# Kernel tuning notes

Measured on AMD Instinct MI355X. Metric: run time of the kernel, lower is better.

Reference implementation:

```python
import jax, jax.numpy as jnp
import numpy as np

D_PRIME = 512
D = 2048
CLASSES = 4


def setup_inputs() -> dict:
    key = jax.random.key(0)
    k1, k2, k3, k4 = jax.random.split(key, 4)
    N = 32768
    V_prime = jax.random.normal(k1, (N, D), dtype=jnp.float32)
    U_t = jax.random.normal(k2, (D_PRIME, D), dtype=jnp.float32)
    W_mta = jax.random.normal(k3, (1, D_PRIME), dtype=jnp.float32)
    W = jax.random.normal(k4, (CLASSES, D), dtype=jnp.float32)
    return {"V_prime": V_prime, "U_t": U_t, "W_mta": W_mta, "W": W}


def reference(V_prime, U_t, W_mta, W):
    # [D_prime, N] = tanh(U_t @ V'^T)
    tanh_scores = jnp.tanh(U_t @ V_prime.T)
    # attention over instances: [1, N]
    a = jax.nn.softmax(W_mta @ tanh_scores, axis=1)
    # weighted sum pooling: [D]
    t = jnp.sum(a.T * V_prime, axis=0)
    # final linear: [1, classes]
    l = (W @ t).reshape(1, CLASSES)
    return l
```

## Files before the change

kernel.cpp:

```cpp
#include <hip/hip_runtime.h>

#define N_INST 32768
#define DIM    2048
#define DP     512
#define NCLS   4

typedef _Float16 half8_t __attribute__((ext_vector_type(8)));
typedef float    float4_t __attribute__((ext_vector_type(4)));

#define OFF_UHI   0ull
#define OFF_S     (OFF_UHI  + (size_t)DP*DIM*2)
#define OFF_STAT  (OFF_S    + (size_t)N_INST*4)
#define OFF_PSTAT (OFF_STAT + 256ull)
#define OFF_PART  (OFF_PSTAT+ 256ull)

__device__ __forceinline__ float tanh_fast(float x) {
  float e = __expf(2.0f * x);
  return 1.0f - 2.0f / (e + 1.0f);
}

__global__ __launch_bounds__(256) void k_cvt(const float4* __restrict__ in,
                                             half8_t* __restrict__ out) {
  int i = blockIdx.x * 256 + threadIdx.x;
  float4 a = in[2 * i], b = in[2 * i + 1];
  half8_t h;
  h[0] = (_Float16)a.x; h[1] = (_Float16)a.y;
  h[2] = (_Float16)a.z; h[3] = (_Float16)a.w;
  h[4] = (_Float16)b.x; h[5] = (_Float16)b.y;
  h[6] = (_Float16)b.z; h[7] = (_Float16)b.w;
  out[i] = h;
}

__global__ __launch_bounds__(256) void k_score_gemm(
    const _Float16* __restrict__ Uhi, const float* __restrict__ V,
    const float* __restrict__ Wmta, float* __restrict__ s) {
  __shared__ _Float16 lA[128 * 32];
  __shared__ _Float16 lB[128 * 32];

  const int tid = threadIdx.x;
  const int lane = tid & 63;
  const int wv = tid >> 6;
  const int waveM = wv >> 1;
  const int waveN = wv & 1;
  const int quad = lane >> 4;
  const int col = lane & 15;

  const int b = blockIdx.x;
  const int grp = b >> 5;
  const int win = b & 31;
  const int mb = win >> 3;
  const int nb = grp * 8 + (win & 7);

  const int aRow0 = mb * 128;
  const int bRow0 = nb * 128;
  const int kStart = (nb & 63) << 5;

  float4_t acc[4][4];
  const float4_t z4 = {0.f, 0.f, 0.f, 0.f};
  for (int i = 0; i < 4; i++)
    for (int j = 0; j < 4; j++) acc[i][j] = z4;

  const int stR = tid >> 2;
  const int stQ = (tid & 3) << 3;

  const _Float16* gA0 = Uhi + (size_t)(aRow0 + stR) * DIM + stQ;
  const _Float16* gA1 = Uhi + (size_t)(aRow0 + 64 + stR) * DIM + stQ;
  const float*    gB0 = V   + (size_t)(bRow0 + stR) * DIM + stQ;
  const float*    gB1 = V   + (size_t)(bRow0 + 64 + stR) * DIM + stQ;

  uint4  ra0, ra1;
  float4 rb0a, rb0b, rb1a, rb1b;

  ra0 = *(const uint4*)(gA0 + kStart);  ra1 = *(const uint4*)(gA1 + kStart);
  rb0a = *(const float4*)(gB0 + kStart);  rb0b = *(const float4*)(gB0 + kStart + 4);
  rb1a = *(const float4*)(gB1 + kStart);  rb1b = *(const float4*)(gB1 + kStart + 4);

  for (int ki = 0; ki < 64; ++ki) {
    __syncthreads();
    *(uint4*)&lA[stR * 32 + stQ] = ra0;
    *(uint4*)&lA[(stR + 64) * 32 + stQ] = ra1;
    {
      half8_t h0, h1;
      h0[0] = (_Float16)rb0a.x; h0[1] = (_Float16)rb0a.y;
      h0[2] = (_Float16)rb0a.z; h0[3] = (_Float16)rb0a.w;
      h0[4] = (_Float16)rb0b.x; h0[5] = (_Float16)rb0b.y;
      h0[6] = (_Float16)rb0b.z; h0[7] = (_Float16)rb0b.w;
      h1[0] = (_Float16)rb1a.x; h1[1] = (_Float16)rb1a.y;
      h1[2] = (_Float16)rb1a.z; h1[3] = (_Float16)rb1a.w;
      h1[4] = (_Float16)rb1b.x; h1[5] = (_Float16)rb1b.y;
      h1[6] = (_Float16)rb1b.z; h1[7] = (_Float16)rb1b.w;
      *(half8_t*)&lB[stR * 32 + stQ] = h0;
      *(half8_t*)&lB[(stR + 64) * 32 + stQ] = h1;
    }
    __syncthreads();

    const int kp = (kStart + (ki + 1) * 32) & (DIM - 1);
    ra0 = *(const uint4*)(gA0 + kp);  ra1 = *(const uint4*)(gA1 + kp);
    rb0a = *(const float4*)(gB0 + kp);  rb0b = *(const float4*)(gB0 + kp + 4);
    rb1a = *(const float4*)(gB1 + kp);  rb1b = *(const float4*)(gB1 + kp + 4);

    half8_t af[4], bf[4];
    for (int mi = 0; mi < 4; mi++) {
      const int row = waveM * 64 + mi * 16 + col;
      af[mi] = *(const half8_t*)&lA[row * 32 + quad * 8];
    }
    for (int ni = 0; ni < 4; ni++) {
      const int row = waveN * 64 + ni * 16 + col;
      bf[ni] = *(const half8_t*)&lB[row * 32 + quad * 8];
    }
    for (int mi = 0; mi < 4; mi++)
      for (int ni = 0; ni < 4; ni++)
        acc[mi][ni] = __builtin_amdgcn_mfma_f32_16x16x32_f16(af[mi], bf[ni], acc[mi][ni], 0, 0, 0);
  }

  for (int ni = 0; ni < 4; ni++) {
    float v = 0.0f;
    for (int mi = 0; mi < 4; mi++) {
      const int jb = aRow0 + waveM * 64 + mi * 16 + quad * 4;
      union { float4_t v4; float f[4]; } u;
      u.v4 = acc[mi][ni];
      for (int r = 0; r < 4; r++)
        v += Wmta[jb + r] * tanh_fast(u.f[r]);
    }
    v += __shfl_xor(v, 16);
    v += __shfl_xor(v, 32);
    if (quad == 0) {
      const int n = bRow0 + waveN * 64 + ni * 16 + col;
      atomicAdd(&s[n], v);
    }
  }
}

__global__ __launch_bounds__(256) void k_stats1(const float* __restrict__ s,
                                                float* __restrict__ pstat) {
  const int tid = threadIdx.x;
  const int lane = tid & 63;
  const int wvi = tid >> 6;
  __shared__ float smM[4], smP[4];
  const float4* s4 = (const float4*)s;

  float4 v = s4[blockIdx.x * 256 + tid];
  float m = fmaxf(fmaxf(v.x, v.y), fmaxf(v.z, v.w));
  float p = __expf(v.x - m) + __expf(v.y - m) + __expf(v.z - m) + __expf(v.w - m);
  for (int o = 32; o > 0; o >>= 1) {
    float om = __shfl_xor(m, o);
    float op = __shfl_xor(p, o);
    float nm = fmaxf(m, om);
    p = p * __expf(m - nm) + op * __expf(om - nm);
    m = nm;
  }
  if (lane == 0) { smM[wvi] = m; smP[wvi] = p; }
  __syncthreads();
  if (tid == 0) {
    float gm = fmaxf(fmaxf(smM[0], smM[1]), fmaxf(smM[2], smM[3]));
    float sum = 0.f;
    for (int w = 0; w < 4; w++) sum += smP[w] * __expf(smM[w] - gm);
    pstat[blockIdx.x * 2]     = gm;
    pstat[blockIdx.x * 2 + 1] = sum;
  }
}

__global__ __launch_bounds__(64) void k_stats2(const float* __restrict__ pstat,
                                               float* __restrict__ stats) {
  const int tid = threadIdx.x;
  float m = -3.4e38f, p = 0.0f;
  if (tid < 32) { m = pstat[tid * 2]; p = pstat[tid * 2 + 1]; }
  for (int o = 32; o > 0; o >>= 1) {
    float om = __shfl_xor(m, o);
    float op = __shfl_xor(p, o);
    float nm = fmaxf(m, om);
    p = p * __expf(m - nm) + op * __expf(om - nm);
    m = nm;
  }
  if (tid == 0) { stats[0] = m; stats[1] = 1.0f / p; }
}

__global__ __launch_bounds__(256) void k_pool(const float* __restrict__ V,
                                              const float* __restrict__ s,
                                              const float* __restrict__ stats,
                                              float* __restrict__ part) {
  const int tid = threadIdx.x;
  const float mx = stats[0], inv = stats[1];
  const int n0 = blockIdx.x * 128;
  float acc[8] = {0.f, 0.f, 0.f, 0.f, 0.f, 0.f, 0.f, 0.f};
  for (int r = 0; r < 128; ++r) {
    const int n = n0 + r;
    const float w = __expf(s[n] - mx) * inv;
    if (w > 1e-12f) {
      const float4* vp = (const float4*)&V[(size_t)n * DIM + tid * 8];
      float4 va = vp[0], vb = vp[1];
      acc[0] += w * va.x; acc[1] += w * va.y; acc[2] += w * va.z; acc[3] += w * va.w;
      acc[4] += w * vb.x; acc[5] += w * vb.y; acc[6] += w * vb.z; acc[7] += w * vb.w;
    }
  }
  float* dst = &part[(size_t)blockIdx.x * DIM + tid * 8];
  *(float4*)(dst + 0) = make_float4(acc[0], acc[1], acc[2], acc[3]);
  *(float4*)(dst + 4) = make_float4(acc[4], acc[5], acc[6], acc[7]);
}

__global__ __launch_bounds__(256) void k_reduce_final(const float* __restrict__ part,
                                                      const float* __restrict__ W,
                                                      float* __restrict__ out) {
  const int d = blockIdx.x * 256 + threadIdx.x;
  float t = 0.f;
  for (int bb = 0; bb < 256; ++bb) t += part[(size_t)bb * DIM + d];

  float pc[NCLS];
#pragma unroll
  for (int c = 0; c < NCLS; ++c) pc[c] = W[(size_t)c * DIM + d] * t;

  __shared__ float sred[4][NCLS];
  const int lane = threadIdx.x & 63;
  const int wvi = threadIdx.x >> 6;
#pragma unroll
  for (int c = 0; c < NCLS; ++c)
    for (int o = 32; o > 0; o >>= 1) pc[c] += __shfl_xor(pc[c], o);
  if (lane == 0)
    for (int c = 0; c < NCLS; ++c) sred[wvi][c] = pc[c];
  __syncthreads();
  if (threadIdx.x < NCLS) {
    float v = sred[0][threadIdx.x] + sred[1][threadIdx.x] +
              sred[2][threadIdx.x] + sred[3][threadIdx.x];
    atomicAdd(&out[threadIdx.x], v);
  }
}

extern "C" void kernel_launch(void* const* d_in, const int* in_sizes, int n_in,
                              void* d_out, int out_size, void* d_ws, size_t ws_size,
                              hipStream_t stream) {
  const float* Vp   = (const float*)d_in[0];
  const float* Ut   = (const float*)d_in[1];
  const float* Wmta = (const float*)d_in[2];
  const float* W    = (const float*)d_in[3];
  float* out = (float*)d_out;

  char* ws = (char*)d_ws;
  _Float16* Uhi  = (_Float16*)(ws + OFF_UHI);
  float*    sBuf = (float*)(ws + OFF_S);
  float*    stat = (float*)(ws + OFF_STAT);
  float*    pstat= (float*)(ws + OFF_PSTAT);
  float*    partB= (float*)(ws + OFF_PART);

  hipMemsetAsync(sBuf, 0, (size_t)N_INST * 4, stream);
  hipMemsetAsync(out, 0, (size_t)NCLS * 4, stream);

  k_cvt<<<(DP * DIM / 8) / 256, 256, 0, stream>>>((const float4*)Ut, (half8_t*)Uhi);
  k_score_gemm<<<(DP / 128) * (N_INST / 128), 256, 0, stream>>>(Uhi, Vp, Wmta, sBuf);
  k_stats1<<<32, 256, 0, stream>>>(sBuf, pstat);
  k_stats2<<<1, 64, 0, stream>>>(pstat, stat);
  k_pool<<<N_INST / 128, 256, 0, stream>>>(Vp, sBuf, stat, partB);
  k_reduce_final<<<DIM / 256, 256, 0, stream>>>(partB, W, out);
}
```

Baseline: 492.1 us.

## Load GEMM tiles directly to LDS and fuse pool reduction via atomics

After: 537.4 us. +9.2%, slower.

```diff
diff --git a/kernel.cpp b/kernel.cpp
--- a/kernel.cpp
+++ b/kernel.cpp
@@ -5,18 +5,24 @@
 #define DP     512
 #define NCLS   4
 
-typedef _Float16 half8_t __attribute__((ext_vector_type(8)));
+typedef _Float16 half8_t  __attribute__((ext_vector_type(8)));
 typedef float    float4_t __attribute__((ext_vector_type(4)));
 
 #define OFF_UHI   0ull
 #define OFF_S     (OFF_UHI  + (size_t)DP*DIM*2)
 #define OFF_STAT  (OFF_S    + (size_t)N_INST*4)
 #define OFF_PSTAT (OFF_STAT + 256ull)
-#define OFF_PART  (OFF_PSTAT+ 256ull)
+#define OFF_T     (OFF_PSTAT+ 256ull)
 
 __device__ __forceinline__ float tanh_fast(float x) {
   float e = __expf(2.0f * x);
   return 1.0f - 2.0f / (e + 1.0f);
+}
+
+typedef const unsigned int __attribute__((address_space(1)))* gas_t;
+typedef unsigned int       __attribute__((address_space(3)))* las_t;
+__device__ __forceinline__ void gl16(const void* g, void* l) {
+  __builtin_amdgcn_global_load_lds((gas_t)g, (las_t)l, 16, 0, 0);
 }
 
 __global__ __launch_bounds__(256) void k_cvt(const float4* __restrict__ in,
@@ -35,90 +41,111 @@
     const _Float16* __restrict__ Uhi, const float* __restrict__ V,
     const float* __restrict__ Wmta, float* __restrict__ s) {
   __shared__ _Float16 lA[128 * 32];
-  __shared__ _Float16 lB[128 * 32];
-
-  const int tid = threadIdx.x;
+  __shared__ float    lB[128 * 32];
+
+  const int tid  = threadIdx.x;
   const int lane = tid & 63;
-  const int wv = tid >> 6;
+  const int wv   = tid >> 6;
   const int waveM = wv >> 1;
   const int waveN = wv & 1;
   const int quad = lane >> 4;
-  const int col = lane & 15;
-
-  const int b = blockIdx.x;
+  const int col  = lane & 15;
+
+  const int b   = blockIdx.x;
   const int grp = b >> 5;
   const int win = b & 31;
-  const int mb = win >> 3;
-  const int nb = grp * 8 + (win & 7);
-
-  const int aRow0 = mb * 128;
-  const int bRow0 = nb * 128;
+  const int mb  = win >> 3;
+  const int nb  = grp * 8 + (win & 7);
+
+  const int aRow0  = mb * 128;
+  const int bRow0  = nb * 128;
   const int kStart = (nb & 63) << 5;
+
+  const int rA0 = wv * 32 + (lane >> 2);
+  const int sA  = (lane & 3) ^ ((rA0 >> 1) & 3);
+  const _Float16* gA0 = Uhi + (size_t)(aRow0 + rA0) * DIM + sA * 8;
+  const _Float16* gA1 = gA0 + (size_t)16 * DIM;
+  _Float16* lAd0 = &lA[(wv * 2 + 0) * 512];
+  _Float16* lAd1 = &lA[(wv * 2 + 1) * 512];
+
+  const int rB0 = wv * 32 + (lane >> 3);
+  const int sB  = (lane & 7) ^ (rB0 & 7);
+  const float* gB0 = V + (size_t)(bRow0 + rB0) * DIM + sB * 4;
+  const float* gB1 = gB0 + (size_t)8  * DIM;
+  const float* gB2 = gB0 + (size_t)16 * DIM;
+  const float* gB3 = gB0 + (size_t)24 * DIM;
+  float* lBd0 = &lB[(wv * 4 + 0) * 256];
+  float* lBd1 = &lB[(wv * 4 + 1) * 256];
+  float* lBd2 = &lB[(wv * 4 + 2) * 256];
+  float* lBd3 = &lB[(wv * 4 + 3) * 256];
+
+  int offA[4];
+#pragma unroll
+  for (int mi = 0; mi < 4; ++mi) {
+    const int r = waveM * 64 + mi * 16 + col;
+    offA[mi] = r * 64 + ((quad ^ ((r >> 1) & 3)) << 4);
+  }
+  int offB[4];
+#pragma unroll
+  for (int ni = 0; ni < 4; ++ni) {
+    const int r = waveN * 64 + ni * 16 + col;
+    offB[ni] = r * 128 + ((((quad << 1)) ^ (r & 7)) << 4);
+  }
 
   float4_t acc[4][4];
   const float4_t z4 = {0.f, 0.f, 0.f, 0.f};
+#pragma unroll
   for (int i = 0; i < 4; i++)
+#pragma unroll
     for (int j = 0; j < 4; j++) acc[i][j] = z4;
 
-  const int stR = tid >> 2;
-  const int stQ = (tid & 3) << 3;
-
-  const _Float16* gA0 = Uhi + (size_t)(aRow0 + stR) * DIM + stQ;
-  const _Float16* gA1 = Uhi + (size_t)(aRow0 + 64 + stR) * DIM + stQ;
-  const float*    gB0 = V   + (size_t)(bRow0 + stR) * DIM + stQ;
-  const float*    gB1 = V   + (size_t)(bRow0 + 64 + stR) * DIM + stQ;
-
-  uint4  ra0, ra1;
-  float4 rb0a, rb0b, rb1a, rb1b;
-
-  ra0 = *(const uint4*)(gA0 + kStart);  ra1 = *(const uint4*)(gA1 + kStart);
-  rb0a = *(const float4*)(gB0 + kStart);  rb0b = *(const float4*)(gB0 + kStart + 4);
-  rb1a = *(const float4*)(gB1 + kStart);  rb1b = *(const float4*)(gB1 + kStart + 4);
+  const char* lAc = (const char*)lA;
+  const char* lBc = (const char*)lB;
 
   for (int ki = 0; ki < 64; ++ki) {
+    const int k = (kStart + (ki << 5)) & (DIM - 1);
     __syncthreads();
-    *(uint4*)&lA[stR * 32 + stQ] = ra0;
-    *(uint4*)&lA[(stR + 64) * 32 + stQ] = ra1;
-    {
-      half8_t h0, h1;
-      h0[0] = (_Float16)rb0a.x; h0[1] = (_Float16)rb0a.y;
-      h0[2] = (_Float16)rb0a.z; h0[3] = (_Float16)rb0a.w;
-      h0[4] = (_Float16)rb0b.x; h0[5] = (_Float16)rb0b.y;
-      h0[6] = (_Float16)rb0b.z; h0[7] = (_Float16)rb0b.w;
-      h1[0] = (_Float16)rb1a.x; h1[1] = (_Float16)rb1a.y;
-      h1[2] = (_Float16)rb1a.z; h1[3] = (_Float16)rb1a.w;
-      h1[4] = (_Float16)rb1b.x; h1[5] = (_Float16)rb1b.y;
-      h1[6] = (_Float16)rb1b.z; h1[7] = (_Float16)rb1b.w;
-      *(half8_t*)&lB[stR * 32 + stQ] = h0;
-      *(half8_t*)&lB[(stR + 64) * 32 + stQ] = h1;
-    }
+    gl16(gA0 + k, lAd0);
+    gl16(gA1 + k, lAd1);
+    gl16(gB0 + k, lBd0);
+    gl16(gB1 + k, lBd1);
+    gl16(gB2 + k, lBd2);
+    gl16(gB3 + k, lBd3);
     __syncthreads();
 
-    const int kp = (kStart + (ki + 1) * 32) & (DIM - 1);
-    ra0 = *(const uint4*)(gA0 + kp);  ra1 = *(const uint4*)(gA1 + kp);
-    rb0a = *(const float4*)(gB0 + kp);  rb0b = *(const float4*)(gB0 + kp + 4);
-    rb1a = *(const float4*)(gB1 + kp);  rb1b = *(const float4*)(gB1 + kp + 4);
-
-    half8_t af[4], bf[4];
-    for (int mi = 0; mi < 4; mi++) {
-      const int row = waveM * 64 + mi * 16 + col;
-      af[mi] = *(const half8_t*)&lA[row * 32 + quad * 8];
-    }
-    for (int ni = 0; ni < 4; ni++) {
-      const int row = waveN * 64 + ni * 16 + col;
-      bf[ni] = *(const half8_t*)&lB[row * 32 + quad * 8];
-    }
-    for (int mi = 0; mi < 4; mi++)
-      for (int ni = 0; ni < 4; ni++)
-        acc[mi][ni] = __builtin_amdgcn_mfma_f32_16x16x32_f16(af[mi], bf[ni], acc[mi][ni], 0, 0, 0);
-  }
-
+    half8_t af[4];
+#pragma unroll
+    for (int mi = 0; mi < 4; ++mi)
+      af[mi] = *(const half8_t*)(lAc + offA[mi]);
+
+#pragma unroll
+    for (int ni = 0; ni < 4; ++ni) {
+      const float4_t x = *(const float4_t*)(lBc + offB[ni]);
+      const float4_t y = *(const float4_t*)(lBc + (offB[ni] ^ 16));
+      const auto c0 = __builtin_amdgcn_cvt_pkrtz(x[0], x[1]);
+      const auto c1 = __builtin_amdgcn_cvt_pkrtz(x[2], x[3]);
+      const auto c2 = __builtin_amdgcn_cvt_pkrtz(y[0], y[1]);
+      const auto c3 = __builtin_amdgcn_cvt_pkrtz(y[2], y[3]);
+      half8_t bf;
+      bf[0] = (_Float16)c0[0]; bf[1] = (_Float16)c0[1];
+      bf[2] = (_Float16)c1[0]; bf[3] = (_Float16)c1[1];
+      bf[4] = (_Float16)c2[0]; bf[5] = (_Float16)c2[1];
+      bf[6] = (_Float16)c3[0]; bf[7] = (_Float16)c3[1];
+#pragma unroll
+      for (int mi = 0; mi < 4; ++mi)
+        acc[mi][ni] = __builtin_amdgcn_mfma_f32_16x16x32_f16(af[mi], bf, acc[mi][ni], 0, 0, 0);
+    }
+  }
+
+#pragma unroll
   for (int ni = 0; ni < 4; ni++) {
     float v = 0.0f;
+#pragma unroll
     for (int mi = 0; mi < 4; mi++) {
       const int jb = aRow0 + waveM * 64 + mi * 16 + quad * 4;
       union { float4_t v4; float f[4]; } u;
       u.v4 = acc[mi][ni];
+#pragma unroll
       for (int r = 0; r < 4; r++)
         v += Wmta[jb + r] * tanh_fast(u.f[r]);
     }
@@ -178,51 +205,61 @@
 __global__ __launch_bounds__(256) void k_pool(const float* __restrict__ V,
                                               const float* __restrict__ s,
                                               const float* __restrict__ stats,
-                                              float* __restrict__ part) {
-  const int tid = threadIdx.x;
+                                              float* __restrict__ t) {
+  __shared__ float wsm[128];
+  __shared__ int hot;
+  const int tid = threadIdx.x;
+  if (tid == 0) hot = 0;
+  __syncthreads();
   const float mx = stats[0], inv = stats[1];
   const int n0 = blockIdx.x * 128;
+  if (tid < 128) {
+    const float w = __expf(s[n0 + tid] - mx) * inv;
+    wsm[tid] = w;
+    if (w > 1e-12f) atomicOr(&hot, 1);
+  }
+  __syncthreads();
+  if (hot == 0) return;
+
   float acc[8] = {0.f, 0.f, 0.f, 0.f, 0.f, 0.f, 0.f, 0.f};
   for (int r = 0; r < 128; ++r) {
-    const int n = n0 + r;
-    const float w = __expf(s[n] - mx) * inv;
+    const float w = wsm[r];
     if (w > 1e-12f) {
-      const float4* vp = (const float4*)&V[(size_t)n * DIM + tid * 8];
+      const float4* vp = (const float4*)&V[(size_t)(n0 + r) * DIM + tid * 8];
       float4 va = vp[0], vb = vp[1];
       acc[0] += w * va.x; acc[1] += w * va.y; acc[2] += w * va.z; acc[3] += w * va.w;
       acc[4] += w * vb.x; acc[5] += w * vb.y; acc[6] += w * vb.z; acc[7] += w * vb.w;
     }
   }
-  float* dst = &part[(size_t)blockIdx.x * DIM + tid * 8];
-  *(float4*)(dst + 0) = make_float4(acc[0], acc[1], acc[2], acc[3]);
-  *(float4*)(dst + 4) = make_float4(acc[4], acc[5], acc[6], acc[7]);
-}
-
-__global__ __launch_bounds__(256) void k_reduce_final(const float* __restrict__ part,
-                                                      const float* __restrict__ W,
-                                                      float* __restrict__ out) {
-  const int d = blockIdx.x * 256 + threadIdx.x;
-  float t = 0.f;
-  for (int bb = 0; bb < 256; ++bb) t += part[(size_t)bb * DIM + d];
-
+#pragma unroll
+  for (int j = 0; j < 8; ++j) atomicAdd(&t[tid * 8 + j], acc[j]);
+}
+
+__global__ __launch_bounds__(256) void k_final(const float* __restrict__ t,
+                                               const float* __restrict__ W,
+                                               float* __restrict__ out) {
+  const int tid = threadIdx.x;
+  const float4* t4 = (const float4*)t;
+  const float4 ta = t4[tid * 2], tb = t4[tid * 2 + 1];
   float pc[NCLS];
 #pragma unroll
-  for (int c = 0; c < NCLS; ++c) pc[c] = W[(size_t)c * DIM + d] * t;
-
+  for (int c = 0; c < NCLS; ++c) {
+    const float4* w4 = (const float4*)&W[(size_t)c * DIM + tid * 8];
+    const float4 wa = w4[0], wb = w4[1];
+    pc[c] = wa.x * ta.x + wa.y * ta.y + wa.z * ta.z + wa.w * ta.w +
+            wb.x * tb.x + wb.y * tb.y + wb.z * tb.z + wb.w * tb.w;
+  }
   __shared__ float sred[4][NCLS];
-  const int lane = threadIdx.x & 63;
-  const int wvi = threadIdx.x >> 6;
+  const int lane = tid & 63, wvi = tid >> 6;
 #pragma unroll
   for (int c = 0; c < NCLS; ++c)
     for (int o = 32; o > 0; o >>= 1) pc[c] += __shfl_xor(pc[c], o);
   if (lane == 0)
+#pragma unroll
     for (int c = 0; c < NCLS; ++c) sred[wvi][c] = pc[c];
   __syncthreads();
-  if (threadIdx.x < NCLS) {
-    float v = sred[0][threadIdx.x] + sred[1][threadIdx.x] +
-              sred[2][threadIdx.x] + sred[3][threadIdx.x];
-    atomicAdd(&out[threadIdx.x], v);
-  }
+  if (tid < NCLS)
+    out[tid] = sred[0][tid] + sred[1][tid] + sred[2][tid] + sred[3][tid];
 }
 
 extern "C" void kernel_launch(void* const* d_in, const int* in_sizes, int n_in,
@@ -239,15 +276,15 @@
   float*    sBuf = (float*)(ws + OFF_S);
   float*    stat = (float*)(ws + OFF_STAT);
   float*    pstat= (float*)(ws + OFF_PSTAT);
-  float*    partB= (float*)(ws + OFF_PART);
+  float*    tvec = (float*)(ws + OFF_T);
 
   hipMemsetAsync(sBuf, 0, (size_t)N_INST * 4, stream);
-  hipMemsetAsync(out, 0, (size_t)NCLS * 4, stream);
+  hipMemsetAsync(tvec, 0, (size_t)DIM * 4, stream);
 
   k_cvt<<<(DP * DIM / 8) / 256, 256, 0, stream>>>((const float4*)Ut, (half8_t*)Uhi);
   k_score_gemm<<<(DP / 128) * (N_INST / 128), 256, 0, stream>>>(Uhi, Vp, Wmta, sBuf);
   k_stats1<<<32, 256, 0, stream>>>(sBuf, pstat);
   k_stats2<<<1, 64, 0, stream>>>(pstat, stat);
-  k_pool<<<N_INST / 128, 256, 0, stream>>>(Vp, sBuf, stat, partB);
-  k_reduce_final<<<DIM / 256, 256, 0, stream>>>(partB, W, out);
-}
+  k_pool<<<N_INST / 128, 256, 0, stream>>>(Vp, sBuf, stat, tvec);
+  k_final<<<1, 256, 0, stream>>>(tvec, W, out);
+}
```
